# Performance work log

Hardware: AMD Instinct MI355X
Metric: run time of the kernel (lower is better)

## Reference

```python
import jax, jax.numpy as jnp
import numpy as np

N, E = 50000, 800000
IN_FEATS, HIDDEN, HEADS, NUM_CLASSES, EDGE_FEAT = 64, 64, 4, 4, 2
D_HEAD = HIDDEN // HEADS


def _lin(key, fan_in, fan_out):
    k1, k2 = jax.random.split(key)
    s = 1.0 / np.sqrt(fan_in)
    W = jax.random.uniform(k1, (fan_in, fan_out), jnp.float32, -s, s)
    b = jax.random.uniform(k2, (fan_out,), jnp.float32, -s, s)
    return W, b


def setup_inputs() -> dict:
    key = jax.random.key(0)
    ks = jax.random.split(key, 10)
    x = jax.random.normal(ks[0], (N, IN_FEATS), jnp.float32)
    edge_index = jax.random.randint(ks[1], (2, E), 0, N, jnp.int32)
    edge_attr = jax.random.normal(ks[2], (E, EDGE_FEAT), jnp.float32)
    Wn, bn = _lin(ks[3], IN_FEATS, HIDDEN)
    We, be = _lin(ks[4], EDGE_FEAT, HIDDEN)
    Wq, bq = _lin(ks[5], HIDDEN, HIDDEN)
    Wk, bk = _lin(ks[6], HIDDEN, HIDDEN)
    Wv, bv = _lin(ks[7], HIDDEN, HIDDEN)
    Ws, bs = _lin(ks[8], HIDDEN, HIDDEN)   # lin_skip (root weight)
    Wf, bf = _lin(ks[9], HIDDEN, NUM_CLASSES)
    return {"x": x, "edge_index": edge_index, "edge_attr": edge_attr,
            "Wn": Wn, "bn": bn, "We": We, "be": be,
            "Wq": Wq, "bq": bq, "Wk": Wk, "bk": bk, "Wv": Wv, "bv": bv,
            "Ws": Ws, "bs": bs, "Wf": Wf, "bf": bf}


def _segment_softmax(logits, seg, num_segments):
    # logits: [E, H], seg: [E] destination node ids
    m = jax.ops.segment_max(logits, seg, num_segments=num_segments)  # [N, H]
    m = jnp.where(jnp.isfinite(m), m, 0.0)
    e = jnp.exp(logits - m[seg])
    s = jax.ops.segment_sum(e, seg, num_segments=num_segments)
    return e / (s[seg] + 1e-16)


def reference(x, edge_index, edge_attr, Wn, bn, We, be, Wq, bq, Wk, bk, Wv, bv, Ws, bs, Wf, bf):
    src, dst = edge_index[0], edge_index[1]
    h = x @ Wn + bn                                   # [N, HIDDEN]
    ea = (edge_attr @ We + be).reshape(E, HEADS, D_HEAD)
    q = (h @ Wq + bq).reshape(N, HEADS, D_HEAD)
    k = (h @ Wk + bk).reshape(N, HEADS, D_HEAD)
    v = (h @ Wv + bv).reshape(N, HEADS, D_HEAD)
    # per-edge attention logits (PyG flow source_to_target: query at dst, key at src)
    logits = jnp.einsum('ehd,ehd->eh', q[dst], k[src]) / np.sqrt(D_HEAD)
    alpha = _segment_softmax(logits, dst, N)          # [E, H]
    # edge_attr added to values (lin_edge is None since edge_dim not set)
    msg = (v[src] + ea) * alpha[:, :, None]           # [E, H, D]
    out = jax.ops.segment_sum(msg, dst, num_segments=N).reshape(N, HIDDEN)
    out = out + h @ Ws + bs                           # root/skip connection
    # dropout is identity in eval mode
    edge_out = out[src] + out[dst]                    # [E, HIDDEN]
    return edge_out @ Wf + bf                         # [E, NUM_CLASSES]
```

## Files before the change

### kernel.cpp

```cpp
#include <hip/hip_runtime.h>
#include <hip/hip_bf16.h>
#include <hip/hip_fp16.h>

#define N_NODES 50000
#define N_EDGES 800000
#define NB_NODE_T ((N_NODES + 31) / 32)
#define NB_ZB ((N_NODES + 255) / 256)
#define WT_BLOCKS 16
#define CAP 64

typedef unsigned short u16;
typedef unsigned int   u32;
typedef __attribute__((ext_vector_type(8))) short short8;
typedef __attribute__((ext_vector_type(4))) float f32x4;

__device__ __forceinline__ float bf2f(u16 u) {
    union { u32 i; float f; } z; z.i = ((u32)u) << 16; return z.f;
}
__device__ __forceinline__ u16 f2bf(float f) {
    union { float f; u32 i; } z; z.f = f;
    u32 x = z.i;
    u32 r = (x + 0x7fffu + ((x >> 16) & 1u)) >> 16;
    return (u16)r;
}
__device__ __forceinline__ float ldf(const void* p, size_t i, bool isbf) {
    return isbf ? bf2f(((const u16*)p)[i]) : ((const float*)p)[i];
}
__device__ __forceinline__ u16 ldbf(const void* p, size_t i, bool isbf) {
    return isbf ? ((const u16*)p)[i] : f2bf(((const float*)p)[i]);
}

#define WSB_COUNT 772

__global__ __launch_bounds__(256) void k_init(
    const void* __restrict__ Wn, const void* __restrict__ bn,
    const void* __restrict__ Wq, const void* __restrict__ bq,
    const void* __restrict__ Wk, const void* __restrict__ bk,
    const void* __restrict__ Wv, const void* __restrict__ bv,
    const void* __restrict__ Ws, const void* __restrict__ bs,
    const void* __restrict__ We, const void* __restrict__ be,
    const void* __restrict__ Wf, const void* __restrict__ bfv,
    u16* __restrict__ wsT, float* __restrict__ wsB,
    int* __restrict__ deg, int* __restrict__ flag)
{
    const int t = threadIdx.x, bid = blockIdx.x;
    if (bid >= WT_BLOCKS) {
        const int idx = (bid - WT_BLOCKS) * 256 + t;
        if (idx < N_NODES) deg[idx] = 0;
        return;
    }
    __shared__ int sflag;
    {
        const u16* p = (const u16*)Wn;
        int found = 0;
        for (int i = t; i < 4096; i += 256) {
            const float v = bf2f(p[i]);
            if (!(fabsf(v) <= 1.0f)) found = 1;
        }
        if (t == 0) sflag = 0;
        __syncthreads();
        if (found) atomicOr(&sflag, 1);
        __syncthreads();
    }
    const bool isbf = (sflag == 0);
    if (bid == 0 && t == 0) flag[0] = sflag;

    const int i = bid * 256 + t;
    {
        const int kk = i >> 6, n = i & 63;
        const int o = n * 64 + kk;
        wsT[0 * 4096 + o] = ldbf(Wn, i, isbf);
        wsT[1 * 4096 + o] = ldbf(Wq, i, isbf);
        wsT[2 * 4096 + o] = ldbf(Wk, i, isbf);
        wsT[3 * 4096 + o] = ldbf(Wv, i, isbf);
        wsT[4 * 4096 + o] = ldbf(Ws, i, isbf);
    }
    if (bid == 0) {
        if (t < 64) {
            wsB[t]       = ldf(bn, t, isbf);
            wsB[64 + t]  = ldf(bq, t, isbf);
            wsB[128 + t] = ldf(bk, t, isbf);
            wsB[192 + t] = ldf(bv, t, isbf);
            wsB[256 + t] = ldf(bs, t, isbf);
            wsB[320 + t] = ldf(We, t, isbf);
            wsB[384 + t] = ldf(We, 64 + t, isbf);
            wsB[448 + t] = ldf(be, t, isbf);
        }
        wsB[512 + t] = ldf(Wf, t, isbf);
        if (t < 4) wsB[768 + t] = ldf(bfv, t, isbf);
    }
}

__global__ __launch_bounds__(512, 4) void k_bn(
    const void* __restrict__ x, const int* __restrict__ ei,
    const void* __restrict__ ea, const int* __restrict__ flag,
    const u16* __restrict__ wsT, const float* __restrict__ wsB,
    int* __restrict__ deg, uint2* __restrict__ rec,
    u16* __restrict__ qbf, u16* __restrict__ kbf, u16* __restrict__ vbf,
    u16* __restrict__ obf)
{
    __shared__ u16 xs[32 * 72];
    const int t = threadIdx.x, bid = blockIdx.x;
    const int w = t >> 6, lane = t & 63;
    const int l15 = lane & 15, quad = lane >> 4;
    const bool isbf = (flag[0] == 0);

    {
        const int e = bid * 512 + t;
        if (e < N_EDGES) {
            const int s = ei[e], d = ei[N_EDGES + e];
            const int rank = atomicAdd(&deg[d], 1) & (CAP - 1);
            float ea0, ea1;
            if (isbf) {
                const u32 w2 = ((const u32*)ea)[e];
                ea0 = bf2f((u16)(w2 & 0xffffu));
                ea1 = bf2f((u16)(w2 >> 16));
            } else {
                const float2 f2 = ((const float2*)ea)[e];
                ea0 = f2.x; ea1 = f2.y;
            }
            const __half2 h = __floats2half2_rn(ea0, ea1);
            uint2 r;
            r.x = (u32)s;
            r.y = *(const u32*)&h;
            rec[((size_t)d << 6) + rank] = r;
        }
    }

    const int base = bid * 32;
    if (t < 256) {
        const int m = t >> 3, kc = t & 7;
        const int node = base + m;
        short8 vd = {0, 0, 0, 0, 0, 0, 0, 0};
        if (node < N_NODES) {
            if (isbf) {
                vd = *(const short8*)((const u16*)x + (size_t)node * 64 + kc * 8);
            } else {
                const float4 f0 = *(const float4*)((const float*)x + (size_t)node * 64 + kc * 8);
                const float4 f1 = *(const float4*)((const float*)x + (size_t)node * 64 + kc * 8 + 4);
                vd[0] = f2bf(f0.x); vd[1] = f2bf(f0.y);
                vd[2] = f2bf(f0.z); vd[3] = f2bf(f0.w);
                vd[4] = f2bf(f1.x); vd[5] = f2bf(f1.y);
                vd[6] = f2bf(f1.z); vd[7] = f2bf(f1.w);
            }
        }
        *(short8*)(xs + m * 72 + kc * 8) = vd;
    }
    short8 b1[2][4];
    if (w < 2) {
        #pragma unroll
        for (int ks = 0; ks < 2; ++ks)
            #pragma unroll
            for (int nt = 0; nt < 4; ++nt)
                b1[ks][nt] = *(const short8*)(wsT + (nt * 16 + l15) * 64 + ks * 32 + quad * 8);
    }
    __syncthreads();

    if (w < 2) {
        f32x4 acc1[4];
        #pragma unroll
        for (int nt = 0; nt < 4; ++nt) acc1[nt] = (f32x4){0.f, 0.f, 0.f, 0.f};
        #pragma unroll
        for (int ks = 0; ks < 2; ++ks) {
            const short8 a = *(const short8*)(xs + (w * 16 + l15) * 72 + ks * 32 + quad * 8);
            #pragma unroll
            for (int nt = 0; nt < 4; ++nt)
                acc1[nt] = __builtin_amdgcn_mfma_f32_16x16x32_bf16(a, b1[ks][nt], acc1[nt], 0, 0, 0);
        }
        #pragma unroll
        for (int nt = 0; nt < 4; ++nt)
            #pragma unroll
            for (int r = 0; r < 4; ++r) {
                const int m = w * 16 + quad * 4 + r;
                const int col = nt * 16 + l15;
                xs[m * 72 + col] = f2bf(acc1[nt][r] + wsB[col]);
            }
    }
    short8 b2[2][4];
    if (w < 4) {
        const u16* wt = wsT + (w + 1) * 4096;
        #pragma unroll
        for (int ks = 0; ks < 2; ++ks)
            #pragma unroll
            for (int nt = 0; nt < 4; ++nt)
                b2[ks][nt] = *(const short8*)(wt + (nt * 16 + l15) * 64 + ks * 32 + quad * 8);
    }
    __syncthreads();

    if (w < 4) {
        f32x4 acc2[2][4];
        #pragma unroll
        for (int mt = 0; mt < 2; ++mt)
            #pragma unroll
            for (int nt = 0; nt < 4; ++nt) acc2[mt][nt] = (f32x4){0.f, 0.f, 0.f, 0.f};
        #pragma unroll
        for (int ks = 0; ks < 2; ++ks) {
            short8 a[2];
            #pragma unroll
            for (int mt = 0; mt < 2; ++mt)
                a[mt] = *(const short8*)(xs + (mt * 16 + l15) * 72 + ks * 32 + quad * 8);
            #pragma unroll
            for (int nt = 0; nt < 4; ++nt)
                #pragma unroll
                for (int mt = 0; mt < 2; ++mt)
                    acc2[mt][nt] = __builtin_amdgcn_mfma_f32_16x16x32_bf16(a[mt], b2[ks][nt], acc2[mt][nt], 0, 0, 0);
        }
        const float* bias = wsB + 64 + w * 64;
        u16* outp = (w == 0) ? qbf : (w == 1) ? kbf : (w == 2) ? vbf : obf;
        #pragma unroll
        for (int mt = 0; mt < 2; ++mt)
            #pragma unroll
            for (int nt = 0; nt < 4; ++nt)
                #pragma unroll
                for (int r = 0; r < 4; ++r) {
                    const int node = base + mt * 16 + quad * 4 + r;
                    if (node >= N_NODES) continue;
                    const int col = nt * 16 + l15;
                    outp[(size_t)node * 64 + col] = f2bf(acc2[mt][nt][r] + bias[col]);
                }
    }
}

__global__ __launch_bounds__(256) void k_agg(
    const int* __restrict__ deg,
    const uint2* __restrict__ rec,
    const u16* __restrict__ qbf, const u16* __restrict__ kbf,
    const u16* __restrict__ vbf, const u16* __restrict__ obf,
    const float* __restrict__ wsB,
    float4* __restrict__ y)
{
    const int wid = (blockIdx.x * 256 + threadIdx.x) >> 6;
    const int lane = threadIdx.x & 63;
    if (wid >= N_NODES) return;
    const int d = wid;
    const int lg = lane & 15;
    const float we0 = wsB[320 + lane];
    const float we1 = wsB[384 + lane];
    const float bef = wsB[448 + lane];
    const ushort4 q4u = *(const ushort4*)(qbf + (size_t)d * 64 + lg * 4);
    const float q0 = bf2f(q4u.x), q1 = bf2f(q4u.y);
    const float q2 = bf2f(q4u.z), q3 = bf2f(q4u.w);
    const float qf = bf2f(qbf[(size_t)d * 64 + lane]);
    const int sb = ((lane >> 4) << 2) + (lane & 3);
    const int beg = d << 6;
    int dg = deg[d];
    dg = (dg > CAP) ? CAP : dg;

    float den = 0.f, accv = 0.f, sa0 = 0.f, sa1 = 0.f;
    int j = 0;
    if (dg >= 4) {
        uint2 rn0 = rec[beg + 0], rn1 = rec[beg + 1];
        uint2 rn2 = rec[beg + 2], rn3 = rec[beg + 3];
        for (; j + 4 <= dg; j += 4) {
            const uint2 r0 = rn0, r1 = rn1, r2 = rn2, r3 = rn3;
            const int g = lane >> 4;
            const u32 smine = (g & 2) ? ((g & 1) ? r3.x : r2.x)
                                      : ((g & 1) ? r1.x : r0.x);
            const ushort4 k4 = *(const ushort4*)(kbf + (size_t)smine * 64 + lg * 4);
            const float v0 = bf2f(vbf[(size_t)(int)r0.x * 64 + lane]);
            const float v1 = bf2f(vbf[(size_t)(int)r1.x * 64 + lane]);
            const float v2 = bf2f(vbf[(size_t)(int)r2.x * 64 + lane]);
            const float v3 = bf2f(vbf[(size_t)(int)r3.x * 64 + lane]);
            const int nb = (j + 8 <= dg) ? (beg + j + 4) : (beg + j);
            rn0 = rec[nb + 0]; rn1 = rec[nb + 1];
            rn2 = rec[nb + 2]; rn3 = rec[nb + 3];
            float prod = q0 * bf2f(k4.x) + q1 * bf2f(k4.y)
                       + q2 * bf2f(k4.z) + q3 * bf2f(k4.w);
            prod += __shfl_xor(prod, 1, 64);
            prod += __shfl_xor(prod, 2, 64);
            const float ex = __expf(prod * 0.25f);
            const float ex0 = __shfl(ex, sb, 64);
            const float ex1 = __shfl(ex, 16 + sb, 64);
            const float ex2 = __shfl(ex, 32 + sb, 64);
            const float ex3 = __shfl(ex, 48 + sb, 64);
            const float2 ea0 = __half22float2(*(const __half2*)&r0.y);
            const float2 ea1 = __half22float2(*(const __half2*)&r1.y);
            const float2 ea2 = __half22float2(*(const __half2*)&r2.y);
            const float2 ea3 = __half22float2(*(const __half2*)&r3.y);
            den  += (ex0 + ex1) + (ex2 + ex3);
            accv += ex0 * v0 + ex1 * v1 + ex2 * v2 + ex3 * v3;
            sa0  += ex0 * ea0.x + ex1 * ea1.x + ex2 * ea2.x + ex3 * ea3.x;
            sa1  += ex0 * ea0.y + ex1 * ea1.y + ex2 * ea2.y + ex3 * ea3.y;
        }
    }
    for (; j < dg; ++j) {
        const uint2 r0 = rec[beg + j];
        const size_t srow = (size_t)(int)r0.x * 64 + lane;
        float prod = qf * bf2f(kbf[srow]);
        prod += __shfl_xor(prod, 1, 64);
        prod += __shfl_xor(prod, 2, 64);
        prod += __shfl_xor(prod, 4, 64);
        prod += __shfl_xor(prod, 8, 64);
        const float ex = __expf(prod * 0.25f);
        const float2 eaf = __half22float2(*(const __half2*)&r0.y);
        den  += ex;
        accv += ex * bf2f(vbf[srow]);
        sa0  += ex * eaf.x;
        sa1  += ex * eaf.y;
    }
    const float num = accv + we0 * sa0 + we1 * sa1 + bef * den;
    const float res = bf2f(obf[(size_t)d * 64 + lane]) + num / (den + 1e-16f);

    float y0 = res * wsB[512 + lane * 4 + 0];
    float y1 = res * wsB[512 + lane * 4 + 1];
    float y2 = res * wsB[512 + lane * 4 + 2];
    float y3 = res * wsB[512 + lane * 4 + 3];
    #pragma unroll
    for (int o = 1; o < 64; o <<= 1) {
        y0 += __shfl_xor(y0, o, 64);
        y1 += __shfl_xor(y1, o, 64);
        y2 += __shfl_xor(y2, o, 64);
        y3 += __shfl_xor(y3, o, 64);
    }
    if (lane == 0) {
        float4 yv;
        yv.x = y0 + 0.5f * wsB[768];
        yv.y = y1 + 0.5f * wsB[769];
        yv.z = y2 + 0.5f * wsB[770];
        yv.w = y3 + 0.5f * wsB[771];
        y[d] = yv;
    }
}

__global__ __launch_bounds__(256) void k_edgeout(
    const int* __restrict__ ei,
    const float4* __restrict__ y,
    const int* __restrict__ flag,
    void* __restrict__ out)
{
    const bool isbf = (flag[0] == 0);
    const int idx = blockIdx.x * 256 + threadIdx.x;
    const int e0 = idx * 2;
    if (e0 >= N_EDGES) return;
    const int2 ss = *(const int2*)(ei + e0);
    const int2 dd = *(const int2*)(ei + N_EDGES + e0);
    const float4 ya = y[ss.x], yb = y[dd.x];
    const float4 yc = y[ss.y], yd = y[dd.y];
    const float a0 = ya.x + yb.x, a1 = ya.y + yb.y;
    const float a2 = ya.z + yb.z, a3 = ya.w + yb.w;
    const float c0 = yc.x + yd.x, c1 = yc.y + yd.y;
    const float c2 = yc.z + yd.z, c3 = yc.w + yd.w;
    if (isbf) {
        uint4 r;
        r.x = (u32)f2bf(a0) | ((u32)f2bf(a1) << 16);
        r.y = (u32)f2bf(a2) | ((u32)f2bf(a3) << 16);
        r.z = (u32)f2bf(c0) | ((u32)f2bf(c1) << 16);
        r.w = (u32)f2bf(c2) | ((u32)f2bf(c3) << 16);
        *(uint4*)((u16*)out + (size_t)e0 * 4) = r;
    } else {
        float4 r0; r0.x = a0; r0.y = a1; r0.z = a2; r0.w = a3;
        float4 r1; r1.x = c0; r1.y = c1; r1.z = c2; r1.w = c3;
        *(float4*)((float*)out + (size_t)e0 * 4) = r0;
        *(float4*)((float*)out + (size_t)e0 * 4 + 4) = r1;
    }
}

extern "C" void kernel_launch(void* const* d_in, const int* in_sizes, int n_in,
                              void* d_out, int out_size, void* d_ws, size_t ws_size,
                              hipStream_t stream)
{
    (void)in_sizes; (void)n_in; (void)out_size; (void)ws_size;
    const void* x   = d_in[0];
    const int*  ei  = (const int*)d_in[1];
    const void* ea  = d_in[2];
    const void* Wn  = d_in[3];  const void* bn  = d_in[4];
    const void* We  = d_in[5];  const void* be  = d_in[6];
    const void* Wq  = d_in[7];  const void* bq  = d_in[8];
    const void* Wk  = d_in[9];  const void* bk  = d_in[10];
    const void* Wv  = d_in[11]; const void* bv  = d_in[12];
    const void* Ws_ = d_in[13]; const void* bs  = d_in[14];
    const void* Wf  = d_in[15]; const void* bfv = d_in[16];

    char*   wsp   = (char*)d_ws;
    uint2*  rec   = (uint2*)wsp;
    float4* y     = (float4*)(rec + (size_t)N_NODES * CAP);
    u16*    qbf   = (u16*)(y + N_NODES);
    u16*    kbf   = qbf + (size_t)N_NODES * 64;
    u16*    vbf   = kbf + (size_t)N_NODES * 64;
    u16*    obf   = vbf + (size_t)N_NODES * 64;
    u16*    wsT   = obf + (size_t)N_NODES * 64;
    float*  wsB   = (float*)(wsT + 5 * 4096);
    int*    deg   = (int*)(wsB + WSB_COUNT);
    int*    flag  = deg + N_NODES;

    k_init<<<WT_BLOCKS + NB_ZB, 256, 0, stream>>>(
        Wn, bn, Wq, bq, Wk, bk, Wv, bv, Ws_, bs, We, be, Wf, bfv,
        wsT, wsB, deg, flag);
    k_bn<<<NB_NODE_T, 512, 0, stream>>>(x, ei, ea, flag, wsT, wsB, deg, rec,
                                        qbf, kbf, vbf, obf);
    k_agg<<<(N_NODES * 64 + 255) / 256, 256, 0, stream>>>(deg, rec, qbf, kbf,
                                                          vbf, obf, wsB, y);
    k_edgeout<<<(N_EDGES / 2 + 255) / 256, 256, 0, stream>>>(ei, y, flag, d_out);
}
```

Measured before the change: 220.9 us.

## Build per-destination edge buckets with range-partitioned LDS counters instead of global atomics

k_init now compresses destination indices to 16-bit, replacing the zeroing of the global degree array. In k_bn, 256 dedicated blocks each own a range of 196 nodes, scan all destinations and bucket their edges using shared-memory atomic counters, then write the degree array directly. This removes contended global atomics and the separate degree zeroing. In exchange, every builder block reads the whole 1.6 MB dst16 array, and the node-transform blocks now process 64 nodes per 512-thread block.

```diff
diff --git a/kernel.cpp b/kernel.cpp
--- a/kernel.cpp
+++ b/kernel.cpp
@@ -4,8 +4,10 @@
 
 #define N_NODES 50000
 #define N_EDGES 800000
-#define NB_NODE_T ((N_NODES + 31) / 32)
-#define NB_ZB ((N_NODES + 255) / 256)
+#define NB_T64 ((N_NODES + 63) / 64)
+#define NB_BUILD 256
+#define RANGE_SZ 196
+#define NB_EP ((N_EDGES / 8 + 255) / 256)
 #define WT_BLOCKS 16
 #define CAP 64
 
@@ -40,13 +42,23 @@
     const void* __restrict__ Ws, const void* __restrict__ bs,
     const void* __restrict__ We, const void* __restrict__ be,
     const void* __restrict__ Wf, const void* __restrict__ bfv,
+    const int* __restrict__ ei,
     u16* __restrict__ wsT, float* __restrict__ wsB,
-    int* __restrict__ deg, int* __restrict__ flag)
+    u16* __restrict__ dst16, int* __restrict__ flag)
 {
     const int t = threadIdx.x, bid = blockIdx.x;
     if (bid >= WT_BLOCKS) {
-        const int idx = (bid - WT_BLOCKS) * 256 + t;
-        if (idx < N_NODES) deg[idx] = 0;
+        const int base8 = ((bid - WT_BLOCKS) * 256 + t) * 8;
+        if (base8 < N_EDGES) {
+            const int4 a = *(const int4*)(ei + N_EDGES + base8);
+            const int4 b = *(const int4*)(ei + N_EDGES + base8 + 4);
+            short8 o;
+            o[0] = (short)a.x; o[1] = (short)a.y;
+            o[2] = (short)a.z; o[3] = (short)a.w;
+            o[4] = (short)b.x; o[5] = (short)b.y;
+            o[6] = (short)b.z; o[7] = (short)b.w;
+            *(short8*)(dst16 + base8) = o;
+        }
         return;
     }
     __shared__ int sflag;
@@ -94,42 +106,63 @@
 __global__ __launch_bounds__(512, 4) void k_bn(
     const void* __restrict__ x, const int* __restrict__ ei,
     const void* __restrict__ ea, const int* __restrict__ flag,
+    const u16* __restrict__ dst16,
     const u16* __restrict__ wsT, const float* __restrict__ wsB,
     int* __restrict__ deg, uint2* __restrict__ rec,
     u16* __restrict__ qbf, u16* __restrict__ kbf, u16* __restrict__ vbf,
     u16* __restrict__ obf)
 {
-    __shared__ u16 xs[32 * 72];
+    __shared__ u16 xs[2 * 32 * 72];
+    __shared__ u32 cnt[RANGE_SZ];
     const int t = threadIdx.x, bid = blockIdx.x;
-    const int w = t >> 6, lane = t & 63;
+    const bool isbf = (flag[0] == 0);
+
+    if (bid < NB_BUILD) {
+        const int lo = bid * RANGE_SZ;
+        const int rsz = (lo + RANGE_SZ <= N_NODES) ? RANGE_SZ : (N_NODES - lo);
+        for (int i = t; i < RANGE_SZ; i += 512) cnt[i] = 0;
+        __syncthreads();
+        const int nch = N_EDGES / 8;
+        for (int c = t; c < nch; c += 512) {
+            const short8 dv = *(const short8*)(dst16 + (size_t)c * 8);
+            #pragma unroll
+            for (int j = 0; j < 8; ++j) {
+                const u32 d = (u16)dv[j];
+                const u32 rel = d - (u32)lo;
+                if (rel < (u32)rsz) {
+                    const int e = c * 8 + j;
+                    const int s = ei[e];
+                    float ea0, ea1;
+                    if (isbf) {
+                        const u32 w2 = ((const u32*)ea)[e];
+                        ea0 = bf2f((u16)(w2 & 0xffffu));
+                        ea1 = bf2f((u16)(w2 >> 16));
+                    } else {
+                        const float2 f2 = ((const float2*)ea)[e];
+                        ea0 = f2.x; ea1 = f2.y;
+                    }
+                    const __half2 h = __floats2half2_rn(ea0, ea1);
+                    const u32 rank = atomicAdd(&cnt[rel], 1u) & (u32)(CAP - 1);
+                    uint2 r;
+                    r.x = (u32)s;
+                    r.y = *(const u32*)&h;
+                    rec[((size_t)d << 6) + rank] = r;
+                }
+            }
+        }
+        __syncthreads();
+        for (int i = t; i < rsz; i += 512) deg[lo + i] = (int)cnt[i];
+        return;
+    }
+
+    const int tt = t & 255, half = t >> 8;
+    const int w = tt >> 6, lane = tt & 63;
     const int l15 = lane & 15, quad = lane >> 4;
-    const bool isbf = (flag[0] == 0);
+    const int base = (bid - NB_BUILD) * 64 + half * 32;
+    u16* xh = xs + half * (32 * 72);
 
     {
-        const int e = bid * 512 + t;
-        if (e < N_EDGES) {
-            const int s = ei[e], d = ei[N_EDGES + e];
-            const int rank = atomicAdd(&deg[d], 1) & (CAP - 1);
-            float ea0, ea1;
-            if (isbf) {
-                const u32 w2 = ((const u32*)ea)[e];
-                ea0 = bf2f((u16)(w2 & 0xffffu));
-                ea1 = bf2f((u16)(w2 >> 16));
-            } else {
-                const float2 f2 = ((const float2*)ea)[e];
-                ea0 = f2.x; ea1 = f2.y;
-            }
-            const __half2 h = __floats2half2_rn(ea0, ea1);
-            uint2 r;
-            r.x = (u32)s;
-            r.y = *(const u32*)&h;
-            rec[((size_t)d << 6) + rank] = r;
-        }
-    }
-
-    const int base = bid * 32;
-    if (t < 256) {
-        const int m = t >> 3, kc = t & 7;
+        const int m = tt >> 3, kc = tt & 7;
         const int node = base + m;
         short8 vd = {0, 0, 0, 0, 0, 0, 0, 0};
         if (node < N_NODES) {
@@ -144,7 +177,7 @@
                 vd[6] = f2bf(f1.z); vd[7] = f2bf(f1.w);
             }
         }
-        *(short8*)(xs + m * 72 + kc * 8) = vd;
+        *(short8*)(xh + m * 72 + kc * 8) = vd;
     }
     short8 b1[2][4];
     if (w < 2) {
@@ -162,7 +195,7 @@
         for (int nt = 0; nt < 4; ++nt) acc1[nt] = (f32x4){0.f, 0.f, 0.f, 0.f};
         #pragma unroll
         for (int ks = 0; ks < 2; ++ks) {
-            const short8 a = *(const short8*)(xs + (w * 16 + l15) * 72 + ks * 32 + quad * 8);
+            const short8 a = *(const short8*)(xh + (w * 16 + l15) * 72 + ks * 32 + quad * 8);
             #pragma unroll
             for (int nt = 0; nt < 4; ++nt)
                 acc1[nt] = __builtin_amdgcn_mfma_f32_16x16x32_bf16(a, b1[ks][nt], acc1[nt], 0, 0, 0);
@@ -173,11 +206,11 @@
             for (int r = 0; r < 4; ++r) {
                 const int m = w * 16 + quad * 4 + r;
                 const int col = nt * 16 + l15;
-                xs[m * 72 + col] = f2bf(acc1[nt][r] + wsB[col]);
+                xh[m * 72 + col] = f2bf(acc1[nt][r] + wsB[col]);
             }
     }
     short8 b2[2][4];
-    if (w < 4) {
+    {
         const u16* wt = wsT + (w + 1) * 4096;
         #pragma unroll
         for (int ks = 0; ks < 2; ++ks)
@@ -187,7 +220,7 @@
     }
     __syncthreads();
 
-    if (w < 4) {
+    {
         f32x4 acc2[2][4];
         #pragma unroll
         for (int mt = 0; mt < 2; ++mt)
@@ -198,7 +231,7 @@
             short8 a[2];
             #pragma unroll
             for (int mt = 0; mt < 2; ++mt)
-                a[mt] = *(const short8*)(xs + (mt * 16 + l15) * 72 + ks * 32 + quad * 8);
+                a[mt] = *(const short8*)(xh + (mt * 16 + l15) * 72 + ks * 32 + quad * 8);
             #pragma unroll
             for (int nt = 0; nt < 4; ++nt)
                 #pragma unroll
@@ -381,13 +414,15 @@
     u16*    wsT   = obf + (size_t)N_NODES * 64;
     float*  wsB   = (float*)(wsT + 5 * 4096);
     int*    deg   = (int*)(wsB + WSB_COUNT);
-    int*    flag  = deg + N_NODES;
-
-    k_init<<<WT_BLOCKS + NB_ZB, 256, 0, stream>>>(
-        Wn, bn, Wq, bq, Wk, bk, Wv, bv, Ws_, bs, We, be, Wf, bfv,
-        wsT, wsB, deg, flag);
-    k_bn<<<NB_NODE_T, 512, 0, stream>>>(x, ei, ea, flag, wsT, wsB, deg, rec,
-                                        qbf, kbf, vbf, obf);
+    u16*    dst16 = (u16*)(deg + N_NODES);
+    int*    flag  = (int*)(dst16 + N_EDGES);
+
+    k_init<<<WT_BLOCKS + NB_EP, 256, 0, stream>>>(
+        Wn, bn, Wq, bq, Wk, bk, Wv, bv, Ws_, bs, We, be, Wf, bfv, ei,
+        wsT, wsB, dst16, flag);
+    k_bn<<<NB_BUILD + NB_T64, 512, 0, stream>>>(x, ei, ea, flag, dst16,
+                                                wsT, wsB, deg, rec,
+                                                qbf, kbf, vbf, obf);
     k_agg<<<(N_NODES * 64 + 255) / 256, 256, 0, stream>>>(deg, rec, qbf, kbf,
                                                           vbf, obf, wsB, y);
     k_edgeout<<<(N_EDGES / 2 + 255) / 256, 256, 0, stream>>>(ei, y, flag, d_out);
```

Result: slower. 350.6 us (+58.7%).
